# Kernel optimization log

Measured on AMD Instinct MI355X. Metric: run time of the kernel, lower is better.

## Reference

```python
import jax, jax.numpy as jnp
import numpy as np
from jax import lax

L, D, H, V = 4, 128, 4, 33
d = D // H  # 32
B, T = 32, 4096

def rms(x, w, eps=1e-5):
    ms = jnp.mean(x.astype(jnp.float32) ** 2, axis=-1, keepdims=True)
    return (x * lax.rsqrt(ms + eps).astype(x.dtype)) * w

def l2n(x, eps=1e-6):
    return x * lax.rsqrt(jnp.sum(x * x, axis=-1, keepdims=True) + eps)

def causal_conv(h, w, b):
    # h: [B,T,D], w: [D,1,K] depthwise, b: [D]; causal via left-pad K-1
    K = w.shape[-1]
    y = lax.conv_general_dilated(h.transpose(0, 2, 1), w, (1,), [(K - 1, 0)],
                                 feature_group_count=h.shape[-1],
                                 dimension_numbers=('NCH', 'OIH', 'NCH'))
    return y.transpose(0, 2, 1) + b

def delta_scan(q, k, v, beta):
    # q,k,v: [B,T,H,d]; beta: [B,T,H]. Rank-1 delta-rule recurrence over T.
    xs = tuple(jnp.moveaxis(a, 1, 0) for a in (q, k, v, beta))
    S0 = jnp.zeros((q.shape[0], q.shape[2], q.shape[3], q.shape[3]), q.dtype)
    def step(S, inp):
        qt, kt, vt, bt = inp
        err = (vt - jnp.einsum('bhij,bhi->bhj', S, kt)) * bt[..., None]
        S = S + kt[..., :, None] * err[..., None, :]
        return S, jnp.einsum('bhij,bhi->bhj', S, qt)
    _, o = lax.scan(step, S0, xs)
    return jnp.moveaxis(o, 0, 1)  # [B,T,H,d]

def setup_inputs() -> dict:
    key = jax.random.key(0)
    ks = iter(jax.random.split(key, 40))
    def rn(shape, scale=0.02):
        return jax.random.normal(next(ks), shape, jnp.float32) * scale
    return {
        'x': jax.random.randint(next(ks), (B, T), 0, V),
        'emb': rn((V, D)),
        'qw': rn((L, D, D)), 'kw': rn((L, D, D)), 'vw': rn((L, D, D)),
        'qcw': rn((L, D, 1, 4), 0.2), 'qcb': rn((L, D)),
        'kcw': rn((L, D, 1, 4), 0.2), 'kcb': rn((L, D)),
        'vcw': rn((L, D, 1, 4), 0.2), 'vcb': rn((L, D)),
        'ow': rn((L, D, D)), 'gw': rn((L, D, D)), 'bw': rn((L, H, D)),
        'hnw': jnp.ones((L, d), jnp.float32),
        'n1w': jnp.ones((L, D), jnp.float32), 'n2w': jnp.ones((L, D), jnp.float32),
        'm1w': rn((L, 2 * D, D)), 'm2w': rn((L, D, 2 * D)),
        'fnw': jnp.ones((D,), jnp.float32), 'hw': rn((V, D)),
    }

def reference(x, emb, qw, kw, vw, qcw, qcb, kcw, kcb, vcw, vcb, ow, gw, bw,
              hnw, n1w, n2w, m1w, m2w, fnw, hw):
    silu = jax.nn.silu
    h = emb[x]  # [B,T,D]
    for l in range(L):
        hn = rms(h, n1w[l])
        q = l2n(silu(causal_conv(hn @ qw[l].T, qcw[l], qcb[l])).reshape(B, T, H, d)) / jnp.sqrt(jnp.float32(d))
        k = l2n(silu(causal_conv(hn @ kw[l].T, kcw[l], kcb[l])).reshape(B, T, H, d))
        v = silu(causal_conv(hn @ vw[l].T, vcw[l], vcb[l])).reshape(B, T, H, d)
        gate = (hn @ gw[l].T).reshape(B, T, H, d)
        beta = jax.nn.sigmoid(hn @ bw[l].T)  # [B,T,H]
        o = delta_scan(q, k, v, beta)
        o = rms(o, hnw[l]) * silu(gate)
        h = h + o.reshape(B, T, D) @ ow[l].T
        h = h + silu(rms(h, n2w[l]) @ m1w[l].T) @ m2w[l].T
    return rms(h, fnw) @ hw.T  # [B,T,V]
```

## Files before the change

kernel.cpp:

```cpp
#include <hip/hip_runtime.h>
#include <hip/hip_bf16.h>
#include <math.h>

#define BB 32
#define TT 4096
#define DD 128
#define HH 4
#define dh 32
#define VV 33
#define LL 4
#define MM (BB*TT)
#define NCHUNK (MM/128)
#define NC 64

typedef short short8 __attribute__((ext_vector_type(8)));
typedef float f32x4 __attribute__((ext_vector_type(4)));

__device__ __forceinline__ float b2f(unsigned short u){
  union{float f; unsigned int x;} v; v.x = ((unsigned int)u)<<16; return v.f;
}
__device__ __forceinline__ unsigned short f2b(float f){
  union{float f; unsigned int x;} v; v.f=f;
  unsigned int r = v.x + 0x7fffu + ((v.x>>16)&1u);
  return (unsigned short)(r>>16);
}
__device__ __forceinline__ float blo(unsigned int u){ union{float f;unsigned int x;}v; v.x=u<<16; return v.f;}
__device__ __forceinline__ float bhi(unsigned int u){ union{float f;unsigned int x;}v; v.x=u&0xffff0000u; return v.f;}
__device__ __forceinline__ float siluf(float x){ return x/(1.0f+expf(-x)); }

__global__ __launch_bounds__(256) void k_embed(const int* __restrict__ x, const float* __restrict__ emb,
                                               float* __restrict__ h){
  int i = blockIdx.x*256 + threadIdx.x;
  int bt = i>>7, c = i&127;
  h[i] = emb[x[bt]*DD + c];
}

__global__ __launch_bounds__(256) void k_rms(const float* __restrict__ src, const float* __restrict__ w,
                                             unsigned short* __restrict__ dst){
  int row = blockIdx.x*4 + (threadIdx.x>>6);
  int lane = threadIdx.x&63;
  const float2 xv = *(const float2*)(src + (size_t)row*DD + lane*2);
  float ss = xv.x*xv.x + xv.y*xv.y;
  #pragma unroll
  for (int m=1;m<64;m<<=1) ss += __shfl_xor(ss,m,64);
  float sc = rsqrtf(ss*(1.0f/128.0f)+1e-5f);
  const float2 wv = *(const float2*)(w + lane*2);
  unsigned int o = ((unsigned int)f2b(xv.y*sc*wv.y)<<16) | (unsigned int)f2b(xv.x*sc*wv.x);
  *(unsigned int*)(dst + (size_t)row*DD + lane*2) = o;
}

template<int ACT, int OUTADD>
__global__ __launch_bounds__(256) void k_gemm(const unsigned short* __restrict__ A,
                                              const float* __restrict__ W,
                                              void* __restrict__ outp, int N, int K){
  __shared__ __align__(16) unsigned short As[128*128];
  __shared__ __align__(16) unsigned short Ws[64*128];
  const int tid = threadIdx.x;
  const int lane = tid & 63, wave = tid >> 6;
  const int row0 = blockIdx.x*128, col0 = blockIdx.y*64;
  const int wr0 = (wave&1)*64, wc0 = (wave>>1)*32;
  const int fr = lane & 15, fq = lane >> 4;
  f32x4 acc[4][2];
  #pragma unroll
  for (int m=0;m<4;m++){
    #pragma unroll
    for (int n=0;n<2;n++) acc[m][n] = (f32x4){0.f,0.f,0.f,0.f};
  }

  for (int kc=0; kc<K; kc+=128){
    #pragma unroll
    for (int ii=0; ii<8; ++ii){
      int flat = tid + ii*256;
      int r = flat>>4, g = flat&15;
      uint4 gv = *(const uint4*)(A + (size_t)(row0+r)*K + kc + g*8);
      *(uint4*)&As[r*128 + ((g^(r&7))<<3)] = gv;
    }
    #pragma unroll
    for (int ii=0; ii<8; ++ii){
      int flat = tid + ii*256;
      int n = flat>>5, q4 = flat&31;
      float4 wv = *(const float4*)(W + (size_t)(col0+n)*K + kc + q4*4);
      uint2 pk;
      pk.x = (unsigned int)f2b(wv.x) | ((unsigned int)f2b(wv.y)<<16);
      pk.y = (unsigned int)f2b(wv.z) | ((unsigned int)f2b(wv.w)<<16);
      int dst = n*128 + ((((q4>>1)^(n&7))<<3) | ((q4&1)<<2));
      *(uint2*)&Ws[dst] = pk;
    }
    __syncthreads();
    #pragma unroll
    for (int ks=0; ks<4; ++ks){
      int gg = ks*4 + fq;
      short8 a[4], b[2];
      #pragma unroll
      for (int m=0;m<4;m++){
        int row = wr0 + m*16 + fr;
        a[m] = *(const short8*)&As[row*128 + ((gg^(row&7))<<3)];
      }
      #pragma unroll
      for (int n=0;n<2;n++){
        int col = wc0 + n*16 + fr;
        b[n] = *(const short8*)&Ws[col*128 + ((gg^(col&7))<<3)];
      }
      #pragma unroll
      for (int m=0;m<4;m++){
        #pragma unroll
        for (int n=0;n<2;n++)
          acc[m][n] = __builtin_amdgcn_mfma_f32_16x16x32_bf16(a[m], b[n], acc[m][n], 0, 0, 0);
      }
    }
    __syncthreads();
  }

  if (OUTADD){
    float* O = (float*)outp;
    #pragma unroll
    for (int m=0;m<4;m++){
      #pragma unroll
      for (int n=0;n<2;n++){
        int ccol = col0 + wc0 + n*16 + fr;
        #pragma unroll
        for (int r=0;r<4;r++){
          int rrow = row0 + wr0 + m*16 + fq*4 + r;
          O[(size_t)rrow*N + ccol] += acc[m][n][r];
        }
      }
    }
  } else {
    unsigned short* O = (unsigned short*)outp;
    #pragma unroll
    for (int m=0;m<4;m++){
      #pragma unroll
      for (int n=0;n<2;n++){
        int ccol = col0 + wc0 + n*16 + fr;
        #pragma unroll
        for (int r=0;r<4;r++){
          int rrow = row0 + wr0 + m*16 + fq*4 + r;
          float vv = acc[m][n][r];
          if (ACT) vv = siluf(vv);
          O[(size_t)rrow*N + ccol] = f2b(vv);
        }
      }
    }
  }
}

__global__ __launch_bounds__(256) void k_beta(const unsigned short* __restrict__ hn,
                                              const float* __restrict__ bwl, float* __restrict__ beta){
  __shared__ unsigned short As[64*128];
  int tid = threadIdx.x; int row0 = blockIdx.x*64;
  #pragma unroll
  for (int ii=0;ii<4;ii++){
    int flat = tid + ii*256;
    int r = flat>>4, v16 = flat&15;
    *(uint4*)&As[r*128 + v16*8] = *(const uint4*)(hn + (size_t)(row0+r)*DD + v16*8);
  }
  __syncthreads();
  int r = tid>>2, n = tid&3;
  const float* wr = bwl + n*DD;
  const unsigned short* ar = &As[r*128];
  float s = 0.f;
  #pragma unroll
  for (int k=0;k<128;k+=8){
    uint4 a = *(const uint4*)(ar + k);
    float4 wa = *(const float4*)(wr + k);
    float4 wb = *(const float4*)(wr + k + 4);
    s += blo(a.x)*wa.x + bhi(a.x)*wa.y + blo(a.y)*wa.z + bhi(a.y)*wa.w;
    s += blo(a.z)*wb.x + bhi(a.z)*wb.y + blo(a.w)*wb.z + bhi(a.w)*wb.w;
  }
  beta[(size_t)(row0+r)*HH + n] = 1.0f/(1.0f+expf(-s));
}

__global__ __launch_bounds__(256) void k_halo(const unsigned short* __restrict__ A,
                                              const unsigned short* __restrict__ B,
                                              const unsigned short* __restrict__ C,
                                              unsigned short* __restrict__ halo){
  int i = blockIdx.x*256 + threadIdx.x;
  int ch = i & 127;
  int rt = i >> 7;
  int r3 = rt % 3;
  int tn = (rt/3) % 3;
  int ck = rt / 9;
  unsigned short v = 0;
  if ((ck & 31) != 0){
    const unsigned short* X = (tn==0) ? A : (tn==1) ? B : C;
    v = X[((size_t)ck*128 - 3 + r3)*DD + ch];
  }
  halo[(size_t)i] = v;
}

__global__ __launch_bounds__(256) void k_conv_ip(
    unsigned short* __restrict__ A, unsigned short* __restrict__ B, unsigned short* __restrict__ C,
    const float* __restrict__ qcw, const float* __restrict__ qcb,
    const float* __restrict__ kcw, const float* __restrict__ kcb,
    const float* __restrict__ vcw, const float* __restrict__ vcb,
    const unsigned short* __restrict__ halo){
  __shared__ __align__(16) unsigned short Xs[131*128];
  const int tid = threadIdx.x;
  const int ck = blockIdx.x, tn = blockIdx.y;
  unsigned short* X = (tn==0) ? A : (tn==1) ? B : C;
  const float* w = (tn==0) ? qcw : (tn==1) ? kcw : vcw;
  const float* bi = (tn==0) ? qcb : (tn==1) ? kcb : vcb;

  if (tid < 48){
    int lr = tid>>4, c16 = tid&15;
    *(uint4*)&Xs[lr*128 + c16*8] = *(const uint4*)&halo[((size_t)(ck*3+tn)*3 + lr)*128 + c16*8];
  }
  #pragma unroll
  for (int ii=0; ii<8; ++ii){
    int flat = tid + ii*256;
    int r = flat>>4, c16 = flat&15;
    *(uint4*)&Xs[(3+r)*128 + c16*8] = *(const uint4*)&X[((size_t)ck*128 + r)*DD + c16*8];
  }
  __syncthreads();

  const int rh = tid>>7, c = tid&127;
  float w0=w[c*4+0], w1=w[c*4+1], w2=w[c*4+2], w3=w[c*4+3];
  float bc = bi[c];
  #pragma unroll 2
  for (int rr=0; rr<64; ++rr){
    int row = rr*2 + rh;
    float y = bc + w0*b2f(Xs[(row+0)*128+c]) + w1*b2f(Xs[(row+1)*128+c])
                 + w2*b2f(Xs[(row+2)*128+c]) + w3*b2f(Xs[(row+3)*128+c]);
    y = siluf(y);
    if (tn < 2){
      float s = y*y;
      #pragma unroll
      for (int m=1;m<32;m<<=1) s += __shfl_xor(s,m,64);
      y *= rsqrtf(s + 1e-6f);
      if (tn==0) y *= 0.17677669529663687f;
    }
    X[((size_t)ck*128 + row)*DD + c] = f2b(y);
  }
}


__global__ __launch_bounds__(256) void k_pA(const unsigned short* __restrict__ kbuf,
                                            unsigned short* vwbuf,
                                            const float* __restrict__ betab,
                                            unsigned short* __restrict__ Ubuf){
  __shared__ float Abt[64][68];
  __shared__ float sol[64][72];
  __shared__ float bs[64];
  const int c = blockIdx.x, bh = blockIdx.y;
  const int b = bh>>2, h = bh&3;
  const int tid = threadIdx.x;
  const int wave = tid>>6, lane = tid&63;
  const int fr = lane&15, fg = lane>>4;
  const size_t base = ((size_t)b*TT + c*64)*128 + h*32;
  const size_t bbase = ((size_t)b*TT + c*64)*4 + h;
  const size_t ub = ((size_t)bh*NC + c)*2048;

  if (tid < 64) bs[tid] = betab[bbase + (size_t)tid*4];

  short8 kA  = *(const short8*)(kbuf + base + (size_t)(wave*16+fr)*128 + fg*8);
  short8 kB0 = *(const short8*)(kbuf + base + (size_t)( 0+fr)*128 + fg*8);
  short8 kB1 = *(const short8*)(kbuf + base + (size_t)(16+fr)*128 + fg*8);
  short8 kB2 = *(const short8*)(kbuf + base + (size_t)(32+fr)*128 + fg*8);
  short8 kB3 = *(const short8*)(kbuf + base + (size_t)(48+fr)*128 + fg*8);
  __syncthreads();

  {
    float4 bsv = *(const float4*)&bs[wave*16 + fg*4];
    f32x4 a;
    #define BUILD(nt, kB) if (wave >= nt){ \
      a = (f32x4){0.f,0.f,0.f,0.f}; \
      a = __builtin_amdgcn_mfma_f32_16x16x32_bf16(kA, kB, a, 0,0,0); \
      Abt[nt*16+fr][wave*16+fg*4+0] = a[0]*bsv.x; \
      Abt[nt*16+fr][wave*16+fg*4+1] = a[1]*bsv.y; \
      Abt[nt*16+fr][wave*16+fg*4+2] = a[2]*bsv.z; \
      Abt[nt*16+fr][wave*16+fg*4+3] = a[3]*bsv.w; }
    BUILD(0, kB0) BUILD(1, kB1) BUILD(2, kB2) BUILD(3, kB3)
    #undef BUILD
  }

  const unsigned short* xp = ((lane<32)? (const unsigned short*)vwbuf : kbuf) + base + (lane&31);
  float racc[16];
  #pragma unroll
  for (int r=0;r<16;r++)
    racc[r] = b2f(xp[(size_t)(wave*16+r)*128]) * bs[wave*16+r];

  #pragma unroll
  for (int p=0;p<4;p++){
    if (wave == p){
      #pragma unroll
      for (int r=0;r<16;r++){
        float w_ = racc[r];
        sol[p*16+r][lane] = w_;
        #pragma unroll
        for (int r2=r+1;r2<16;r2++)
          racc[r2] -= Abt[p*16+r][p*16+r2] * w_;
      }
    }
    __syncthreads();
    if (wave > p){
      #pragma unroll
      for (int s16=0;s16<16;s16++){
        float w_ = sol[p*16+s16][lane];
        #pragma unroll
        for (int r=0;r<16;r++)
          racc[r] -= Abt[p*16+s16][wave*16+r] * w_;
      }
    }
    __syncthreads();
  }

  {
    int row = tid>>2, qt = tid&3;
    if (qt < 2){
      #pragma unroll
      for (int i=0;i<8;i++){
        int col = qt*16 + i*2;
        unsigned int pk = (unsigned int)f2b(sol[row][col]) | ((unsigned int)f2b(sol[row][col+1])<<16);
        *(unsigned int*)(vwbuf + base + (size_t)row*128 + col) = pk;
      }
    } else {
      #pragma unroll
      for (int i=0;i<8;i++){
        int col = (qt-2)*16 + i*2;
        unsigned int pk = (unsigned int)f2b(sol[row][32+col]) | ((unsigned int)f2b(sol[row][33+col])<<16);
        *(unsigned int*)(Ubuf + ub + row*32 + col) = pk;
      }
    }
  }
}

template<int PREC>
__global__ __launch_bounds__(64) void k_pB(const unsigned short* __restrict__ kbuf,
                                           unsigned short* webuf,
                                           const unsigned short* __restrict__ Ubuf,
                                           void* __restrict__ SentP){
  __shared__ float Sl[32][33];
  __shared__ unsigned short El[64][40];
  __shared__ unsigned short Ell[64][40];
  __shared__ unsigned short Kl[64][40];
  const int bh = blockIdx.x, b = bh>>2, h = bh&3;
  const int lane = threadIdx.x, fr = lane&15, fg = lane>>4;
  for (int i=lane; i<32*33; i+=64) ((float*)Sl)[i] = 0.f;
  f32x4 sc[2][2];
  #pragma unroll
  for (int it=0;it<2;it++){
    #pragma unroll
    for (int ct=0;ct<2;ct++) sc[it][ct]=(f32x4){0.f,0.f,0.f,0.f};
  }

  for (int c=0;c<NC;c++){
    const size_t base = ((size_t)b*TT + c*64)*128 + h*32;
    const size_t ub = ((size_t)bh*NC + c)*2048;
    {
      const unsigned short* kr = kbuf + base + (size_t)lane*128;
      const unsigned short* wr = webuf + base + (size_t)lane*128;
      uint4 a0=*(const uint4*)(kr),   a1=*(const uint4*)(kr+8);
      uint4 a2=*(const uint4*)(kr+16),a3=*(const uint4*)(kr+24);
      uint4 b0=*(const uint4*)(wr),   b1=*(const uint4*)(wr+8);
      uint4 b2=*(const uint4*)(wr+16),b3=*(const uint4*)(wr+24);
      *(uint4*)&Kl[lane][0]=a0; *(uint4*)&Kl[lane][8]=a1;
      *(uint4*)&Kl[lane][16]=a2; *(uint4*)&Kl[lane][24]=a3;
      *(uint4*)&El[lane][0]=b0; *(uint4*)&El[lane][8]=b1;
      *(uint4*)&El[lane][16]=b2; *(uint4*)&El[lane][24]=b3;
    }
    short8 uf[4];
    #pragma unroll
    for (int mt=0;mt<4;mt++)
      uf[mt] = *(const short8*)(Ubuf + ub + (size_t)(mt*16+fr)*32 + fg*8);
    f32x4 acc[4][2];
    #pragma unroll
    for (int mt=0;mt<4;mt++){
      #pragma unroll
      for (int ct=0;ct<2;ct++){
        #pragma unroll
        for (int r=0;r<4;r++)
          acc[mt][ct][r] = b2f(El[mt*16+fg*4+r][ct*16+fr]);
      }
    }
    short8 sb[2], sbl[2];
    #pragma unroll
    for (int ct=0;ct<2;ct++){
      short8 neg, negl;
      float pos[8];
      #pragma unroll
      for (int jj=0;jj<8;jj++){
        float sv = Sl[fg*8+jj][ct*16+fr];
        pos[jj] = sv;
        float nv = -sv;
        unsigned short hi = f2b(nv);
        neg[jj]=(short)hi;
        negl[jj]=(short)f2b(nv - b2f(hi));
      }
      sb[ct]=neg; sbl[ct]=negl;
      if (PREC){
        float* Sf = (float*)SentP + ((size_t)bh*NC + c)*1024 + ct*512 + lane*8;
        *(float4*)Sf     = (float4){pos[0],pos[1],pos[2],pos[3]};
        *(float4*)(Sf+4) = (float4){pos[4],pos[5],pos[6],pos[7]};
      } else {
        short8 p8;
        #pragma unroll
        for (int jj=0;jj<8;jj++) p8[jj]=(short)f2b(pos[jj]);
        *(short8*)((unsigned short*)SentP + ((size_t)bh*NC + c)*1024 + ct*512 + lane*8) = p8;
      }
    }
    #pragma unroll
    for (int mt=0;mt<4;mt++){
      #pragma unroll
      for (int ct=0;ct<2;ct++){
        acc[mt][ct] = __builtin_amdgcn_mfma_f32_16x16x32_bf16(uf[mt], sb[ct],  acc[mt][ct],0,0,0);
        acc[mt][ct] = __builtin_amdgcn_mfma_f32_16x16x32_bf16(uf[mt], sbl[ct], acc[mt][ct],0,0,0);
      }
    }
    #pragma unroll
    for (int mt=0;mt<4;mt++){
      #pragma unroll
      for (int ct=0;ct<2;ct++){
        #pragma unroll
        for (int r=0;r<4;r++){
          float ef = acc[mt][ct][r];
          unsigned short eh = f2b(ef);
          int t = mt*16+fg*4+r, j = ct*16+fr;
          El[t][j] = eh;
          Ell[t][j] = f2b(ef - b2f(eh));
          webuf[base + (size_t)t*128 + j] = eh;
        }
      }
    }
    short8 ka[2][2], eb[2][2], ebl[2][2];
    #pragma unroll
    for (int it=0;it<2;it++){
      #pragma unroll
      for (int ks=0;ks<2;ks++){
        short8 tmp;
        #pragma unroll
        for (int jj=0;jj<8;jj++) tmp[jj] = (short)Kl[ks*32+fg*8+jj][it*16+fr];
        ka[it][ks]=tmp;
      }
    }
    #pragma unroll
    for (int ct=0;ct<2;ct++){
      #pragma unroll
      for (int ks=0;ks<2;ks++){
        short8 t1v, t2v;
        #pragma unroll
        for (int jj=0;jj<8;jj++){
          t1v[jj] = (short)El[ks*32+fg*8+jj][ct*16+fr];
          t2v[jj] = (short)Ell[ks*32+fg*8+jj][ct*16+fr];
        }
        eb[ct][ks]=t1v; ebl[ct][ks]=t2v;
      }
    }
    #pragma unroll
    for (int it=0;it<2;it++){
      #pragma unroll
      for (int ct=0;ct<2;ct++){
        #pragma unroll
        for (int ks=0;ks<2;ks++){
          sc[it][ct] = __builtin_amdgcn_mfma_f32_16x16x32_bf16(ka[it][ks], eb[ct][ks],  sc[it][ct],0,0,0);
          sc[it][ct] = __builtin_amdgcn_mfma_f32_16x16x32_bf16(ka[it][ks], ebl[ct][ks], sc[it][ct],0,0,0);
        }
      }
    }
    #pragma unroll
    for (int it=0;it<2;it++){
      #pragma unroll
      for (int ct=0;ct<2;ct++){
        #pragma unroll
        for (int r=0;r<4;r++)
          Sl[it*16+fg*4+r][ct*16+fr] = sc[it][ct][r];
      }
    }
  }
}

template<int PREC>
__global__ __launch_bounds__(64) void k_pC(unsigned short* qobuf,
                                           const unsigned short* __restrict__ kbuf,
                                           const unsigned short* __restrict__ ebuf,
                                           const void* __restrict__ SentP){
  __shared__ unsigned short Pl[64][72];
  __shared__ unsigned short Plo[64][72];
  __shared__ unsigned short El[64][40];
  const int c = blockIdx.x, bh = blockIdx.y, b=bh>>2, h=bh&3;
  const int lane=threadIdx.x, fr=lane&15, fg=lane>>4;
  const size_t base = ((size_t)b*TT + c*64)*128 + h*32;
  #pragma unroll
  for (int i=0;i<9;i++){
    *(uint4*)&Pl[lane][i*8]  = (uint4){0u,0u,0u,0u};
    *(uint4*)&Plo[lane][i*8] = (uint4){0u,0u,0u,0u};
  }
  {
    const unsigned short* er = ebuf + base + (size_t)lane*128;
    uint4 a0=*(const uint4*)(er),   a1=*(const uint4*)(er+8);
    uint4 a2=*(const uint4*)(er+16),a3=*(const uint4*)(er+24);
    *(uint4*)&El[lane][0]=a0; *(uint4*)&El[lane][8]=a1;
    *(uint4*)&El[lane][16]=a2; *(uint4*)&El[lane][24]=a3;
  }
  short8 qf[4], kf[4];
  #pragma unroll
  for (int mt=0;mt<4;mt++){
    qf[mt] = *(const short8*)(qobuf + base + (size_t)(mt*16+fr)*128 + fg*8);
    kf[mt] = *(const short8*)(kbuf  + base + (size_t)(mt*16+fr)*128 + fg*8);
  }
  #pragma unroll
  for (int mt=0;mt<4;mt++){
    #pragma unroll
    for (int nt=0;nt<4;nt++){
      if (nt>mt) continue;
      f32x4 p = (f32x4){0.f,0.f,0.f,0.f};
      p = __builtin_amdgcn_mfma_f32_16x16x32_bf16(qf[mt], kf[nt], p,0,0,0);
      #pragma unroll
      for (int r=0;r<4;r++){
        int t = mt*16+fg*4+r, s = nt*16+fr;
        float pv = p[r];
        unsigned short ph = f2b(pv);
        Pl[t][s]  = (s<=t)? ph : (unsigned short)0;
        Plo[t][s] = (s<=t)? f2b(pv - b2f(ph)) : (unsigned short)0;
      }
    }
  }
  f32x4 acc[4][2];
  #pragma unroll
  for (int mt=0;mt<4;mt++){
    #pragma unroll
    for (int ct=0;ct<2;ct++) acc[mt][ct]=(f32x4){0.f,0.f,0.f,0.f};
  }
  if (PREC){
    short8 sfh[2], sfl[2];
    #pragma unroll
    for (int ct=0;ct<2;ct++){
      const float* Sf = (const float*)SentP + ((size_t)bh*NC + c)*1024 + ct*512 + lane*8;
      float4 v0 = *(const float4*)Sf;
      float4 v1 = *(const float4*)(Sf+4);
      float sv[8] = {v0.x,v0.y,v0.z,v0.w,v1.x,v1.y,v1.z,v1.w};
      short8 hh, ll;
      #pragma unroll
      for (int jj=0;jj<8;jj++){
        unsigned short hi = f2b(sv[jj]);
        hh[jj]=(short)hi; ll[jj]=(short)f2b(sv[jj]-b2f(hi));
      }
      sfh[ct]=hh; sfl[ct]=ll;
    }
    #pragma unroll
    for (int mt=0;mt<4;mt++){
      #pragma unroll
      for (int ct=0;ct<2;ct++){
        acc[mt][ct]=__builtin_amdgcn_mfma_f32_16x16x32_bf16(qf[mt], sfh[ct], acc[mt][ct],0,0,0);
        acc[mt][ct]=__builtin_amdgcn_mfma_f32_16x16x32_bf16(qf[mt], sfl[ct], acc[mt][ct],0,0,0);
      }
    }
  } else {
    short8 sf[2];
    #pragma unroll
    for (int ct=0;ct<2;ct++)
      sf[ct] = *(const short8*)((const unsigned short*)SentP + ((size_t)bh*NC + c)*1024 + ct*512 + lane*8);
    #pragma unroll
    for (int mt=0;mt<4;mt++){
      #pragma unroll
      for (int ct=0;ct<2;ct++)
        acc[mt][ct]=__builtin_amdgcn_mfma_f32_16x16x32_bf16(qf[mt], sf[ct], acc[mt][ct],0,0,0);
    }
  }
  short8 ebf[2][2];
  #pragma unroll
  for (int ct=0;ct<2;ct++){
    #pragma unroll
    for (int ks=0;ks<2;ks++){
      short8 tmp;
      #pragma unroll
      for (int jj=0;jj<8;jj++) tmp[jj]=(short)El[ks*32+fg*8+jj][ct*16+fr];
      ebf[ct][ks]=tmp;
    }
  }
  #pragma unroll
  for (int mt=0;mt<4;mt++){
    #pragma unroll
    for (int ks=0;ks<2;ks++){
      short8 pa  = *(const short8*)&Pl[mt*16+fr][ks*32+fg*8];
      short8 pal = *(const short8*)&Plo[mt*16+fr][ks*32+fg*8];
      #pragma unroll
      for (int ct=0;ct<2;ct++){
        acc[mt][ct]=__builtin_amdgcn_mfma_f32_16x16x32_bf16(pa,  ebf[ct][ks], acc[mt][ct],0,0,0);
        acc[mt][ct]=__builtin_amdgcn_mfma_f32_16x16x32_bf16(pal, ebf[ct][ks], acc[mt][ct],0,0,0);
      }
    }
  }
  #pragma unroll
  for (int mt=0;mt<4;mt++){
    #pragma unroll
    for (int ct=0;ct<2;ct++){
      #pragma unroll
      for (int r=0;r<4;r++)
        qobuf[base + (size_t)(mt*16+fg*4+r)*128 + ct*16+fr] = f2b(acc[mt][ct][r]);
    }
  }
}

__global__ __launch_bounds__(64) void k_scan(const unsigned short* q, const unsigned short* k,
                                             const unsigned short* v, const float* beta,
                                             unsigned short* o){
  int b = blockIdx.x>>2, hh = blockIdx.x&3;
  int lane = threadIdx.x;
  int j = lane&31, ih = lane>>5;
  float S[16];
  #pragma unroll
  for (int m=0;m<16;m++) S[m]=0.f;
  size_t idx0 = ((size_t)b*TT*HH + hh)*dh;
  size_t bidx0 = (size_t)b*TT*HH + hh;
  const unsigned short* kp = k + idx0 + ih*16;
  const unsigned short* qp = q + idx0 + ih*16;
  for (int t=0;t<TT;t++){
    size_t ofs=(size_t)t*128;
    uint4 ka=*(const uint4*)(kp+ofs), kb=*(const uint4*)(kp+ofs+8);
    uint4 qa=*(const uint4*)(qp+ofs), qb=*(const uint4*)(qp+ofs+8);
    float kf[16], qf[16];
    kf[0]=blo(ka.x);kf[1]=bhi(ka.x);kf[2]=blo(ka.y);kf[3]=bhi(ka.y);
    kf[4]=blo(ka.z);kf[5]=bhi(ka.z);kf[6]=blo(ka.w);kf[7]=bhi(ka.w);
    kf[8]=blo(kb.x);kf[9]=bhi(kb.x);kf[10]=blo(kb.y);kf[11]=bhi(kb.y);
    kf[12]=blo(kb.z);kf[13]=bhi(kb.z);kf[14]=blo(kb.w);kf[15]=bhi(kb.w);
    qf[0]=blo(qa.x);qf[1]=bhi(qa.x);qf[2]=blo(qa.y);qf[3]=bhi(qa.y);
    qf[4]=blo(qa.z);qf[5]=bhi(qa.z);qf[6]=blo(qa.w);qf[7]=bhi(qa.w);
    qf[8]=blo(qb.x);qf[9]=bhi(qb.x);qf[10]=blo(qb.y);qf[11]=bhi(qb.y);
    qf[12]=blo(qb.z);qf[13]=bhi(qb.z);qf[14]=blo(qb.w);qf[15]=bhi(qb.w);
    float vc = b2f(v[idx0+ofs+j]), bc = beta[bidx0+(size_t)t*4];
    float p0=0,p1=0,p2=0,p3=0;
    #pragma unroll
    for (int m=0;m<4;m++){
      p0 += S[m]*kf[m]; p1 += S[m+4]*kf[m+4]; p2 += S[m+8]*kf[m+8]; p3 += S[m+12]*kf[m+12];
    }
    float p = (p0+p1)+(p2+p3);
    p += __shfl_xor(p, 32, 64);
    float err = (vc - p)*bc;
    float o0=0,o1=0,o2=0,o3=0;
    #pragma unroll
    for (int m=0;m<4;m++){
      S[m]    += kf[m]*err;     o0 += S[m]*qf[m];
      S[m+4]  += kf[m+4]*err;   o1 += S[m+4]*qf[m+4];
      S[m+8]  += kf[m+8]*err;   o2 += S[m+8]*qf[m+8];
      S[m+12] += kf[m+12]*err;  o3 += S[m+12]*qf[m+12];
    }
    float oo = (o0+o1)+(o2+o3);
    oo += __shfl_xor(oo, 32, 64);
    if (ih==0) o[idx0 + ofs + j] = f2b(oo);
  }
}

__global__ __launch_bounds__(256) void k_ogate(const unsigned short* __restrict__ o, const unsigned short* __restrict__ gate,
                                               const float* __restrict__ hnwl, unsigned short* __restrict__ tmp){
  int tid=threadIdx.x;
  size_t bt = (size_t)blockIdx.x*2 + (tid>>7);
  int c = tid&127;
  size_t i = bt*DD + c;
  float ov = b2f(o[i]);
  float ss = ov*ov;
  #pragma unroll
  for (int m=1;m<32;m<<=1) ss += __shfl_xor(ss,m,64);
  float r = rsqrtf(ss*(1.0f/32.0f)+1e-5f);
  float g = b2f(gate[i]);
  tmp[i] = f2b(ov*r*hnwl[c&31]*siluf(g));
}

__global__ __launch_bounds__(256) void k_head(const unsigned short* __restrict__ hf, const float* __restrict__ hw,
                                              float* __restrict__ out){
  int gid = blockIdx.x*256+threadIdx.x;
  if (gid >= MM*VV) return;
  int row = gid/VV, n = gid - row*VV;
  const unsigned short* a = hf + (size_t)row*DD;
  const float* w = hw + n*DD;
  float s=0.f;
  #pragma unroll
  for (int k2=0;k2<128;k2+=8){
    uint4 av = *(const uint4*)(a+k2);
    float4 wa = *(const float4*)(w+k2);
    float4 wb = *(const float4*)(w+k2+4);
    s += blo(av.x)*wa.x + bhi(av.x)*wa.y + blo(av.y)*wa.z + bhi(av.y)*wa.w;
    s += blo(av.z)*wb.x + bhi(av.z)*wb.y + blo(av.w)*wb.z + bhi(av.w)*wb.w;
  }
  out[gid] = s;
}

extern "C" void kernel_launch(void* const* d_in, const int* in_sizes, int n_in,
                              void* d_out, int out_size, void* d_ws, size_t ws_size,
                              hipStream_t stream){
  const int*   x   = (const int*)d_in[0];
  const float* emb = (const float*)d_in[1];
  const float* qw  = (const float*)d_in[2];
  const float* kw  = (const float*)d_in[3];
  const float* vw  = (const float*)d_in[4];
  const float* qcw = (const float*)d_in[5];
  const float* qcb = (const float*)d_in[6];
  const float* kcw = (const float*)d_in[7];
  const float* kcb = (const float*)d_in[8];
  const float* vcw = (const float*)d_in[9];
  const float* vcb = (const float*)d_in[10];
  const float* ow  = (const float*)d_in[11];
  const float* gw  = (const float*)d_in[12];
  const float* bw  = (const float*)d_in[13];
  const float* hnw = (const float*)d_in[14];
  const float* n1w = (const float*)d_in[15];
  const float* n2w = (const float*)d_in[16];
  const float* m1w = (const float*)d_in[17];
  const float* m2w = (const float*)d_in[18];
  const float* fnw = (const float*)d_in[19];
  const float* hw  = (const float*)d_in[20];

  char* ws = (char*)d_ws;
  size_t off = 0;
  float* h             = (float*)(ws+off);          off += (size_t)MM*DD*4;
  unsigned short* hn   = (unsigned short*)(ws+off); off += (size_t)MM*DD*2;
  unsigned short* A    = (unsigned short*)(ws+off); off += (size_t)MM*DD*2;
  unsigned short* B    = (unsigned short*)(ws+off); off += (size_t)MM*DD*2;
  unsigned short* C    = (unsigned short*)(ws+off); off += (size_t)MM*DD*2;
  float* beta          = (float*)(ws+off);          off += (size_t)MM*HH*4;
  unsigned short* halo = (unsigned short*)(ws+off); off += (size_t)NCHUNK*9*128*2;
  unsigned short* U    = (unsigned short*)(ws+off); off += (size_t)MM*DD*2;
  void* SentP          = (void*)(ws+off);
  const size_t NEED1 = off + (size_t)8192*1024*4;
  const size_t NEED0 = off + (size_t)8192*1024*2;
  unsigned short* t1   = A;
  const int mode = (ws_size >= NEED1) ? 1 : (ws_size >= NEED0) ? 0 : -1;

  k_embed<<<MM*DD/256, 256, 0, stream>>>(x, emb, h);
  for (int l=0;l<LL;l++){
    k_rms<<<MM/4,256,0,stream>>>(h, n1w + l*DD, hn);
    k_gemm<0,0><<<dim3(MM/128,2),256,0,stream>>>(hn, qw + l*DD*DD, A, 128, 128);
    k_gemm<0,0><<<dim3(MM/128,2),256,0,stream>>>(hn, kw + l*DD*DD, B, 128, 128);
    k_gemm<0,0><<<dim3(MM/128,2),256,0,stream>>>(hn, vw + l*DD*DD, C, 128, 128);
    k_beta<<<MM/64,256,0,stream>>>(hn, bw + l*HH*DD, beta);
    k_halo<<<NCHUNK*9*128/256,256,0,stream>>>(A, B, C, halo);
    k_conv_ip<<<dim3(NCHUNK,3),256,0,stream>>>(A, B, C,
                                  qcw+l*DD*4, qcb+l*DD, kcw+l*DD*4, kcb+l*DD, vcw+l*DD*4, vcb+l*DD,
                                  halo);
    if (mode >= 0){
      k_pA<<<dim3(NC, BB*HH), 256, 0, stream>>>(B, C, beta, U);
      if (mode==1){
        k_pB<1><<<BB*HH, 64, 0, stream>>>(B, C, U, SentP);
        k_pC<1><<<dim3(NC, BB*HH), 64, 0, stream>>>(A, B, C, SentP);
      } else {
        k_pB<0><<<BB*HH, 64, 0, stream>>>(B, C, U, SentP);
        k_pC<0><<<dim3(NC, BB*HH), 64, 0, stream>>>(A, B, C, SentP);
      }
    } else {
      k_scan<<<BB*HH,64,0,stream>>>(A, B, C, beta, A);
    }
    k_gemm<0,0><<<dim3(MM/128,2),256,0,stream>>>(hn, gw + l*DD*DD, C, 128, 128);
    k_ogate<<<MM/2,256,0,stream>>>(A, C, hnw+l*dh, B);
    k_gemm<0,1><<<dim3(MM/128,2),256,0,stream>>>(B, ow + l*DD*DD, h, 128, 128);
    k_rms<<<MM/4,256,0,stream>>>(h, n2w + l*DD, hn);
    k_gemm<1,0><<<dim3(MM/128,4),256,0,stream>>>(hn, m1w + l*2*DD*DD, t1, 256, 128);
    k_gemm<0,1><<<dim3(MM/128,2),256,0,stream>>>(t1, m2w + l*2*DD*DD, h, 128, 256);
  }
  k_rms<<<MM/4,256,0,stream>>>(h, fnw, hn);
  k_head<<<(MM*VV+255)/256,256,0,stream>>>(hn, hw, (float*)d_out);
}
```

Baseline: 3.297 ms.

## Reuse staged A tile across column panels and move LM head to MFMA

The GEMM kernel now processes NP=2 column panels of 64 per block. The staged A tile is loaded into shared memory once and reused for both panels, so each row block reads the activation matrix half as often and the grid is halved. The scalar per-output LM head kernel is replaced by an MFMA tile kernel that pads the vocab dimension to 64 and masks the stores. The cost is twice the accumulator registers, an extra sync per panel, and wasted MFMA work on the padded vocab columns.

```diff
diff --git a/kernel.cpp b/kernel.cpp
--- a/kernel.cpp
+++ b/kernel.cpp
@@ -49,7 +49,7 @@
   *(unsigned int*)(dst + (size_t)row*DD + lane*2) = o;
 }
 
-template<int ACT, int OUTADD>
+template<int NP, int ACT, int OUTADD>
 __global__ __launch_bounds__(256) void k_gemm(const unsigned short* __restrict__ A,
                                               const float* __restrict__ W,
                                               void* __restrict__ outp, int N, int K){
@@ -57,15 +57,16 @@
   __shared__ __align__(16) unsigned short Ws[64*128];
   const int tid = threadIdx.x;
   const int lane = tid & 63, wave = tid >> 6;
-  const int row0 = blockIdx.x*128, col0 = blockIdx.y*64;
+  const int row0 = blockIdx.x*128, colbase = blockIdx.y*(64*NP);
   const int wr0 = (wave&1)*64, wc0 = (wave>>1)*32;
   const int fr = lane & 15, fq = lane >> 4;
-  f32x4 acc[4][2];
-  #pragma unroll
-  for (int m=0;m<4;m++){
-    #pragma unroll
-    for (int n=0;n<2;n++) acc[m][n] = (f32x4){0.f,0.f,0.f,0.f};
-  }
+  f32x4 acc[NP][4][2];
+  #pragma unroll
+  for (int p=0;p<NP;p++)
+    #pragma unroll
+    for (int m=0;m<4;m++)
+      #pragma unroll
+      for (int n=0;n<2;n++) acc[p][m][n] = (f32x4){0.f,0.f,0.f,0.f};
 
   for (int kc=0; kc<K; kc+=128){
     #pragma unroll
@@ -76,68 +77,149 @@
       *(uint4*)&As[r*128 + ((g^(r&7))<<3)] = gv;
     }
     #pragma unroll
-    for (int ii=0; ii<8; ++ii){
-      int flat = tid + ii*256;
-      int n = flat>>5, q4 = flat&31;
-      float4 wv = *(const float4*)(W + (size_t)(col0+n)*K + kc + q4*4);
-      uint2 pk;
-      pk.x = (unsigned int)f2b(wv.x) | ((unsigned int)f2b(wv.y)<<16);
-      pk.y = (unsigned int)f2b(wv.z) | ((unsigned int)f2b(wv.w)<<16);
-      int dst = n*128 + ((((q4>>1)^(n&7))<<3) | ((q4&1)<<2));
-      *(uint2*)&Ws[dst] = pk;
-    }
-    __syncthreads();
-    #pragma unroll
-    for (int ks=0; ks<4; ++ks){
-      int gg = ks*4 + fq;
-      short8 a[4], b[2];
+    for (int p=0;p<NP;p++){
+      const int col0 = colbase + p*64;
+      #pragma unroll
+      for (int ii=0; ii<8; ++ii){
+        int flat = tid + ii*256;
+        int n = flat>>5, q4 = flat&31;
+        float4 wv = *(const float4*)(W + (size_t)(col0+n)*K + kc + q4*4);
+        uint2 pk;
+        pk.x = (unsigned int)f2b(wv.x) | ((unsigned int)f2b(wv.y)<<16);
+        pk.y = (unsigned int)f2b(wv.z) | ((unsigned int)f2b(wv.w)<<16);
+        int dst = n*128 + ((((q4>>1)^(n&7))<<3) | ((q4&1)<<2));
+        *(uint2*)&Ws[dst] = pk;
+      }
+      __syncthreads();
+      #pragma unroll
+      for (int ks=0; ks<4; ++ks){
+        int gg = ks*4 + fq;
+        short8 a[4], b[2];
+        #pragma unroll
+        for (int m=0;m<4;m++){
+          int row = wr0 + m*16 + fr;
+          a[m] = *(const short8*)&As[row*128 + ((gg^(row&7))<<3)];
+        }
+        #pragma unroll
+        for (int n=0;n<2;n++){
+          int col = wc0 + n*16 + fr;
+          b[n] = *(const short8*)&Ws[col*128 + ((gg^(col&7))<<3)];
+        }
+        #pragma unroll
+        for (int m=0;m<4;m++){
+          #pragma unroll
+          for (int n=0;n<2;n++)
+            acc[p][m][n] = __builtin_amdgcn_mfma_f32_16x16x32_bf16(a[m], b[n], acc[p][m][n], 0, 0, 0);
+        }
+      }
+      __syncthreads();
+    }
+  }
+
+  #pragma unroll
+  for (int p=0;p<NP;p++){
+    const int col0 = colbase + p*64;
+    if (OUTADD){
+      float* O = (float*)outp;
       #pragma unroll
       for (int m=0;m<4;m++){
-        int row = wr0 + m*16 + fr;
-        a[m] = *(const short8*)&As[row*128 + ((gg^(row&7))<<3)];
-      }
-      #pragma unroll
-      for (int n=0;n<2;n++){
-        int col = wc0 + n*16 + fr;
-        b[n] = *(const short8*)&Ws[col*128 + ((gg^(col&7))<<3)];
-      }
+        #pragma unroll
+        for (int n=0;n<2;n++){
+          int ccol = col0 + wc0 + n*16 + fr;
+          #pragma unroll
+          for (int r=0;r<4;r++){
+            int rrow = row0 + wr0 + m*16 + fq*4 + r;
+            O[(size_t)rrow*N + ccol] += acc[p][m][n][r];
+          }
+        }
+      }
+    } else {
+      unsigned short* O = (unsigned short*)outp;
       #pragma unroll
       for (int m=0;m<4;m++){
         #pragma unroll
-        for (int n=0;n<2;n++)
-          acc[m][n] = __builtin_amdgcn_mfma_f32_16x16x32_bf16(a[m], b[n], acc[m][n], 0, 0, 0);
-      }
-    }
-    __syncthreads();
-  }
-
-  if (OUTADD){
-    float* O = (float*)outp;
+        for (int n=0;n<2;n++){
+          int ccol = col0 + wc0 + n*16 + fr;
+          #pragma unroll
+          for (int r=0;r<4;r++){
+            int rrow = row0 + wr0 + m*16 + fq*4 + r;
+            float vv = acc[p][m][n][r];
+            if (ACT) vv = siluf(vv);
+            O[(size_t)rrow*N + ccol] = f2b(vv);
+          }
+        }
+      }
+    }
+  }
+}
+
+__global__ __launch_bounds__(256) void k_headm(const unsigned short* __restrict__ A,
+                                               const float* __restrict__ W,
+                                               float* __restrict__ out){
+  __shared__ __align__(16) unsigned short As[128*128];
+  __shared__ __align__(16) unsigned short Ws[64*128];
+  const int tid = threadIdx.x;
+  const int lane = tid & 63, wave = tid >> 6;
+  const int row0 = blockIdx.x*128;
+  const int wr0 = (wave&1)*64, wc0 = (wave>>1)*32;
+  const int fr = lane & 15, fq = lane >> 4;
+  f32x4 acc[4][2];
+  #pragma unroll
+  for (int m=0;m<4;m++)
+    #pragma unroll
+    for (int n=0;n<2;n++) acc[m][n] = (f32x4){0.f,0.f,0.f,0.f};
+
+  #pragma unroll
+  for (int ii=0; ii<8; ++ii){
+    int flat = tid + ii*256;
+    int r = flat>>4, g = flat&15;
+    uint4 gv = *(const uint4*)(A + (size_t)(row0+r)*DD + g*8);
+    *(uint4*)&As[r*128 + ((g^(r&7))<<3)] = gv;
+  }
+  #pragma unroll
+  for (int ii=0; ii<8; ++ii){
+    int flat = tid + ii*256;
+    int n = flat>>5, q4 = flat&31;
+    float4 wv = (n < VV) ? *(const float4*)(W + (size_t)n*DD + q4*4)
+                         : (float4){0.f,0.f,0.f,0.f};
+    uint2 pk;
+    pk.x = (unsigned int)f2b(wv.x) | ((unsigned int)f2b(wv.y)<<16);
+    pk.y = (unsigned int)f2b(wv.z) | ((unsigned int)f2b(wv.w)<<16);
+    int dst = n*128 + ((((q4>>1)^(n&7))<<3) | ((q4&1)<<2));
+    *(uint2*)&Ws[dst] = pk;
+  }
+  __syncthreads();
+  #pragma unroll
+  for (int ks=0; ks<4; ++ks){
+    int gg = ks*4 + fq;
+    short8 a[4], b[2];
     #pragma unroll
     for (int m=0;m<4;m++){
-      #pragma unroll
-      for (int n=0;n<2;n++){
-        int ccol = col0 + wc0 + n*16 + fr;
+      int row = wr0 + m*16 + fr;
+      a[m] = *(const short8*)&As[row*128 + ((gg^(row&7))<<3)];
+    }
+    #pragma unroll
+    for (int n=0;n<2;n++){
+      int col = wc0 + n*16 + fr;
+      b[n] = *(const short8*)&Ws[col*128 + ((gg^(col&7))<<3)];
+    }
+    #pragma unroll
+    for (int m=0;m<4;m++){
+      #pragma unroll
+      for (int n=0;n<2;n++)
+        acc[m][n] = __builtin_amdgcn_mfma_f32_16x16x32_bf16(a[m], b[n], acc[m][n], 0, 0, 0);
+    }
+  }
+  #pragma unroll
+  for (int m=0;m<4;m++){
+    #pragma unroll
+    for (int n=0;n<2;n++){
+      int ccol = wc0 + n*16 + fr;
+      if (ccol < VV){
         #pragma unroll
         for (int r=0;r<4;r++){
           int rrow = row0 + wr0 + m*16 + fq*4 + r;
-          O[(size_t)rrow*N + ccol] += acc[m][n][r];
-        }
-      }
-    }
-  } else {
-    unsigned short* O = (unsigned short*)outp;
-    #pragma unroll
-    for (int m=0;m<4;m++){
-      #pragma unroll
-      for (int n=0;n<2;n++){
-        int ccol = col0 + wc0 + n*16 + fr;
-        #pragma unroll
-        for (int r=0;r<4;r++){
-          int rrow = row0 + wr0 + m*16 + fq*4 + r;
-          float vv = acc[m][n][r];
-          if (ACT) vv = siluf(vv);
-          O[(size_t)rrow*N + ccol] = f2b(vv);
+          out[(size_t)rrow*VV + ccol] = acc[m][n][r];
         }
       }
     }
@@ -232,7 +314,6 @@
     X[((size_t)ck*128 + row)*DD + c] = f2b(y);
   }
 }
-
 
 __global__ __launch_bounds__(256) void k_pA(const unsigned short* __restrict__ kbuf,
                                             unsigned short* vwbuf,
@@ -653,25 +734,6 @@
   float r = rsqrtf(ss*(1.0f/32.0f)+1e-5f);
   float g = b2f(gate[i]);
   tmp[i] = f2b(ov*r*hnwl[c&31]*siluf(g));
-}
-
-__global__ __launch_bounds__(256) void k_head(const unsigned short* __restrict__ hf, const float* __restrict__ hw,
-                                              float* __restrict__ out){
-  int gid = blockIdx.x*256+threadIdx.x;
-  if (gid >= MM*VV) return;
-  int row = gid/VV, n = gid - row*VV;
-  const unsigned short* a = hf + (size_t)row*DD;
-  const float* w = hw + n*DD;
-  float s=0.f;
-  #pragma unroll
-  for (int k2=0;k2<128;k2+=8){
-    uint4 av = *(const uint4*)(a+k2);
-    float4 wa = *(const float4*)(w+k2);
-    float4 wb = *(const float4*)(w+k2+4);
-    s += blo(av.x)*wa.x + bhi(av.x)*wa.y + blo(av.y)*wa.z + bhi(av.y)*wa.w;
-    s += blo(av.z)*wb.x + bhi(av.z)*wb.y + blo(av.w)*wb.z + bhi(av.w)*wb.w;
-  }
-  out[gid] = s;
 }
 
 extern "C" void kernel_launch(void* const* d_in, const int* in_sizes, int n_in,
@@ -718,9 +780,9 @@
   k_embed<<<MM*DD/256, 256, 0, stream>>>(x, emb, h);
   for (int l=0;l<LL;l++){
     k_rms<<<MM/4,256,0,stream>>>(h, n1w + l*DD, hn);
-    k_gemm<0,0><<<dim3(MM/128,2),256,0,stream>>>(hn, qw + l*DD*DD, A, 128, 128);
-    k_gemm<0,0><<<dim3(MM/128,2),256,0,stream>>>(hn, kw + l*DD*DD, B, 128, 128);
-    k_gemm<0,0><<<dim3(MM/128,2),256,0,stream>>>(hn, vw + l*DD*DD, C, 128, 128);
+    k_gemm<2,0,0><<<dim3(MM/128,1),256,0,stream>>>(hn, qw + l*DD*DD, A, 128, 128);
+    k_gemm<2,0,0><<<dim3(MM/128,1),256,0,stream>>>(hn, kw + l*DD*DD, B, 128, 128);
+    k_gemm<2,0,0><<<dim3(MM/128,1),256,0,stream>>>(hn, vw + l*DD*DD, C, 128, 128);
     k_beta<<<MM/64,256,0,stream>>>(hn, bw + l*HH*DD, beta);
     k_halo<<<NCHUNK*9*128/256,256,0,stream>>>(A, B, C, halo);
     k_conv_ip<<<dim3(NCHUNK,3),256,0,stream>>>(A, B, C,
@@ -738,13 +800,13 @@
     } else {
       k_scan<<<BB*HH,64,0,stream>>>(A, B, C, beta, A);
     }
-    k_gemm<0,0><<<dim3(MM/128,2),256,0,stream>>>(hn, gw + l*DD*DD, C, 128, 128);
+    k_gemm<2,0,0><<<dim3(MM/128,1),256,0,stream>>>(hn, gw + l*DD*DD, C, 128, 128);
     k_ogate<<<MM/2,256,0,stream>>>(A, C, hnw+l*dh, B);
-    k_gemm<0,1><<<dim3(MM/128,2),256,0,stream>>>(B, ow + l*DD*DD, h, 128, 128);
+    k_gemm<2,0,1><<<dim3(MM/128,1),256,0,stream>>>(B, ow + l*DD*DD, h, 128, 128);
     k_rms<<<MM/4,256,0,stream>>>(h, n2w + l*DD, hn);
-    k_gemm<1,0><<<dim3(MM/128,4),256,0,stream>>>(hn, m1w + l*2*DD*DD, t1, 256, 128);
-    k_gemm<0,1><<<dim3(MM/128,2),256,0,stream>>>(t1, m2w + l*2*DD*DD, h, 128, 256);
+    k_gemm<2,1,0><<<dim3(MM/128,2),256,0,stream>>>(hn, m1w + l*2*DD*DD, t1, 256, 128);
+    k_gemm<2,0,1><<<dim3(MM/128,1),256,0,stream>>>(t1, m2w + l*2*DD*DD, h, 128, 256);
   }
   k_rms<<<MM/4,256,0,stream>>>(h, fnw, hn);
-  k_head<<<(MM*VV+255)/256,256,0,stream>>>(hn, hw, (float*)d_out);
-}
+  k_headm<<<MM/128,256,0,stream>>>(hn, hw, (float*)d_out);
+}
```

Result: faster. 2.831 ms (-14.1%).
